# Kernel optimization log

Measured on AMD Instinct MI355X. Metric: run time of the kernel, lower is better.

The kernel has to match this reference:

```python
import jax, jax.numpy as jnp
import numpy as np

IN_FEATURES = 4096
OUT_FEATURES = 4096
SPARSITY = 0.98


def _build_mask():
    # Mirrors _initialize_structured_sparsity: banded deterministic pattern.
    num_connections = int((1 - SPARSITY) * IN_FEATURES * OUT_FEATURES)
    cpn = max(1, num_connections // OUT_FEATURES)  # connections per neuron (=81)
    rows = np.arange(OUT_FEATURES)[:, None]                      # [O,1]
    cols = (rows * cpn + np.arange(cpn)[None, :]) % IN_FEATURES  # [O,cpn]
    mask = np.zeros((OUT_FEATURES, IN_FEATURES), dtype=np.float32)
    mask[np.repeat(np.arange(OUT_FEATURES), cpn), cols.reshape(-1)] = 1.0
    return mask, cpn


def setup_inputs() -> dict:
    key = jax.random.key(0)
    kx, kw = jax.random.split(key)
    mask_np, cpn = _build_mask()
    x = jax.random.normal(kx, (16384, IN_FEATURES), dtype=jnp.float32)
    # weight init: randn * sqrt(2/cpn) at masked positions (dense tensor is fine;
    # forward multiplies by mask anyway, matching the torch module exactly)
    weight = jax.random.normal(kw, (OUT_FEATURES, IN_FEATURES), dtype=jnp.float32) * jnp.float32(np.sqrt(2.0 / cpn))
    bias = jnp.zeros((OUT_FEATURES,), dtype=jnp.float32)
    mask = jnp.asarray(mask_np)
    return {"x": x, "weight": weight, "bias": bias, "mask": mask}


def reference(x, weight, bias, mask):
    # F.linear(x, weight*mask, bias) == x @ (weight*mask).T + bias
    masked_weight = weight * mask  # [O,I]
    return jnp.einsum('bi,oi->bo', x, masked_weight) + bias
```

## Files before the change

### kernel.cpp

```cpp
#include <hip/hip_runtime.h>
#include <hip/hip_bf16.h>

#define IN_F 4096
#define OUT_F 4096
#define CPN 81
#define OINV 2225
#define OB16 2832

#define BMF 8
#define NCH 8
#define CHUNK 512
#define SC4 148
#define XSTR 616
#define RSTRF 8

typedef __attribute__((ext_vector_type(4))) float f32x4;
typedef __attribute__((ext_vector_type(8))) short bf16x8;

__device__ __forceinline__ unsigned short f2bf(float f) {
  __hip_bfloat16 h = __float2bfloat16(f);
  return *reinterpret_cast<unsigned short*>(&h);
}
__device__ __forceinline__ float bf2f(unsigned short u) {
  unsigned int v = ((unsigned int)u) << 16;
  return *reinterpret_cast<float*>(&v);
}

__global__ void prep_wfrag(const float* __restrict__ w,
                           const float* __restrict__ mask,
                           unsigned short* __restrict__ wfrag) {
  int idx = blockIdx.x * 256 + threadIdx.x;
  int lane = idx & 63;
  int t = (idx >> 6) % 3;
  int g = idx / 192;
  int n = lane & 15;
  int kg = lane >> 4;
  int s = g * 16 + n;
  int o = (OINV * s) & 4095;
  unsigned short v8[8];
#pragma unroll
  for (int i = 0; i < 8; ++i) {
    int c = 32 * t + 8 * kg + i;
    int j = c - n;
    float v = 0.f;
    if (j >= 0 && j < CPN) {
      int col = (16 * g + c) & 4095;
      v = w[(size_t)o * IN_F + col] * mask[(size_t)o * IN_F + col];
    }
    v8[i] = f2bf(v);
  }
  *reinterpret_cast<bf16x8*>(wfrag + (size_t)idx * 8) =
      *reinterpret_cast<const bf16x8*>(v8);
}

__global__ __launch_bounds__(512, 4) void sc_fused(
    const float* __restrict__ x, const float* __restrict__ bias,
    const unsigned short* __restrict__ wfrag, float* __restrict__ out) {
  __shared__ unsigned short res[4096 * RSTRF];
  __shared__ unsigned short xl[BMF * XSTR];

  const int blk = blockIdx.x;
  const int b0 = blk * BMF;
  const int tid = threadIdx.x;
  const int wave = tid >> 6;
  const int lane = tid & 63;
  const int ln = lane & 15;
  const int lk = lane >> 4;
  const int oln = (OINV * ln) & 4095;
  const int q0 = blk & 7;

  for (int qq = 0; qq < NCH; ++qq) {
    const int q = (q0 + qq) & 7;
    const int c0 = q * CHUNK;

#pragma unroll
    for (int k = 0; k < 3; ++k) {
      int idx = tid + k * 512;
      if (idx < BMF * SC4) {
        int row = idx / SC4;
        int c4 = idx - row * SC4;
        int col = (c0 + 4 * c4) & 4095;
        const float4 v = *reinterpret_cast<const float4*>(
            x + (size_t)(b0 + row) * IN_F + col);
        ushort4 h;
        h.x = f2bf(v.x); h.y = f2bf(v.y); h.z = f2bf(v.z); h.w = f2bf(v.w);
        *reinterpret_cast<ushort4*>(xl + row * XSTR + 4 * c4) = h;
      }
    }
    __syncthreads();

    const unsigned short* arow = xl + (ln & 7) * XSTR + 8 * lk;
#pragma unroll
    for (int j = 0; j < 4; ++j) {
      const int gl = wave * 4 + j;
      const int g = q * 32 + gl;
      const bf16x8* wf = reinterpret_cast<const bf16x8*>(wfrag)
                       + (size_t)g * 192 + lane;
      const unsigned short* ap = arow + 16 * gl;
      bf16x8 a0 = *reinterpret_cast<const bf16x8*>(ap);
      bf16x8 a1 = *reinterpret_cast<const bf16x8*>(ap + 32);
      bf16x8 a2 = *reinterpret_cast<const bf16x8*>(ap + 64);
      f32x4 acc = f32x4{0.f, 0.f, 0.f, 0.f};
      acc = __builtin_amdgcn_mfma_f32_16x16x32_bf16(a0, wf[0],   acc, 0, 0, 0);
      acc = __builtin_amdgcn_mfma_f32_16x16x32_bf16(a1, wf[64],  acc, 0, 0, 0);
      acc = __builtin_amdgcn_mfma_f32_16x16x32_bf16(a2, wf[128], acc, 0, 0, 0);
      if (lk < 2) {
        int o = (OB16 * g + oln) & 4095;
        ushort4 h;
        h.x = f2bf(acc[0]); h.y = f2bf(acc[1]);
        h.z = f2bf(acc[2]); h.w = f2bf(acc[3]);
        *reinterpret_cast<ushort4*>(res + o * RSTRF + 4 * lk) = h;
      }
    }
    __syncthreads();
  }

  const int h8 = tid >> 8;
  const int c = tid & 255;
#pragma unroll 4
  for (int i = 0; i < 16; ++i) {
    int o = i * 256 + c;
    const uint2 v = *reinterpret_cast<const uint2*>(res + o * RSTRF + 4 * h8);
    float b = bias[o];
    float r0 = bf2f((unsigned short)(v.x & 0xffff)) + b;
    float r1 = bf2f((unsigned short)(v.x >> 16)) + b;
    float r2 = bf2f((unsigned short)(v.y & 0xffff)) + b;
    float r3 = bf2f((unsigned short)(v.y >> 16)) + b;
    size_t base = (size_t)(b0 + 4 * h8) * OUT_F + o;
    out[base]             = r0;
    out[base + OUT_F]     = r1;
    out[base + 2 * OUT_F] = r2;
    out[base + 3 * OUT_F] = r3;
  }
}

extern "C" void kernel_launch(void* const* d_in, const int* in_sizes, int n_in,
                              void* d_out, int out_size, void* d_ws, size_t ws_size,
                              hipStream_t stream) {
  const float* x    = (const float*)d_in[0];
  const float* w    = (const float*)d_in[1];
  const float* bias = (const float*)d_in[2];
  const float* mask = (const float*)d_in[3];
  float* out = (float*)d_out;

  unsigned short* wfrag = (unsigned short*)d_ws;

  const int B = in_sizes[0] / IN_F;

  prep_wfrag<<<192, 256, 0, stream>>>(w, mask, wfrag);
  sc_fused<<<B / BMF, 512, 0, stream>>>(x, bias, wfrag, out);
}
```

Before: 191.1 us.

## Prefetch next x chunk into registers and double-buffer weight fragment loads

Loads the next chunk of x into registers right after the barrier so global latency overlaps the MFMA work, and software-pipelines the weight and LDS fragment loads across the four inner groups. It also changes the epilogue mapping so each wave writes 16 consecutive outputs for pairs of rows instead of 4 rows per thread. This raises register pressure under the 512x4 launch bounds, and the new store pattern writes 16 consecutive floats per row per wave, which may coalesce worse.

```diff
diff --git a/kernel.cpp b/kernel.cpp
--- a/kernel.cpp
+++ b/kernel.cpp
@@ -11,6 +11,7 @@
 #define NCH 8
 #define CHUNK 512
 #define SC4 148
+#define NLD 1184
 #define XSTR 616
 #define RSTRF 8
 
@@ -69,43 +70,75 @@
   const int oln = (OINV * ln) & 4095;
   const int q0 = blk & 7;
 
+  const int i1 = tid + 512, i2 = tid + 1024;
+  const int row0 = tid / SC4, c40 = tid - row0 * SC4;
+  const int row1 = i1  / SC4, c41 = i1  - row1 * SC4;
+  const int row2 = i2  / SC4, c42 = i2  - row2 * SC4;
+  const bool v2 = (i2 < NLD);
+  const float* xp0 = x + (size_t)(b0 + row0) * IN_F;
+  const float* xp1 = x + (size_t)(b0 + row1) * IN_F;
+  const float* xp2 = x + (size_t)(b0 + row2) * IN_F;
+  unsigned short* xw0 = xl + row0 * XSTR + 4 * c40;
+  unsigned short* xw1 = xl + row1 * XSTR + 4 * c41;
+  unsigned short* xw2 = xl + row2 * XSTR + 4 * c42;
+
+  float4 xr0, xr1, xr2;
+  {
+    const int c0 = q0 * CHUNK;
+    xr0 = *reinterpret_cast<const float4*>(xp0 + ((c0 + 4 * c40) & 4095));
+    xr1 = *reinterpret_cast<const float4*>(xp1 + ((c0 + 4 * c41) & 4095));
+    if (v2) xr2 = *reinterpret_cast<const float4*>(xp2 + ((c0 + 4 * c42) & 4095));
+  }
+
   for (int qq = 0; qq < NCH; ++qq) {
     const int q = (q0 + qq) & 7;
-    const int c0 = q * CHUNK;
 
-#pragma unroll
-    for (int k = 0; k < 3; ++k) {
-      int idx = tid + k * 512;
-      if (idx < BMF * SC4) {
-        int row = idx / SC4;
-        int c4 = idx - row * SC4;
-        int col = (c0 + 4 * c4) & 4095;
-        const float4 v = *reinterpret_cast<const float4*>(
-            x + (size_t)(b0 + row) * IN_F + col);
-        ushort4 h;
-        h.x = f2bf(v.x); h.y = f2bf(v.y); h.z = f2bf(v.z); h.w = f2bf(v.w);
-        *reinterpret_cast<ushort4*>(xl + row * XSTR + 4 * c4) = h;
+    {
+      ushort4 h;
+      h.x = f2bf(xr0.x); h.y = f2bf(xr0.y); h.z = f2bf(xr0.z); h.w = f2bf(xr0.w);
+      *reinterpret_cast<ushort4*>(xw0) = h;
+      h.x = f2bf(xr1.x); h.y = f2bf(xr1.y); h.z = f2bf(xr1.z); h.w = f2bf(xr1.w);
+      *reinterpret_cast<ushort4*>(xw1) = h;
+      if (v2) {
+        h.x = f2bf(xr2.x); h.y = f2bf(xr2.y); h.z = f2bf(xr2.z); h.w = f2bf(xr2.w);
+        *reinterpret_cast<ushort4*>(xw2) = h;
       }
     }
     __syncthreads();
 
-    const unsigned short* arow = xl + (ln & 7) * XSTR + 8 * lk;
+    if (qq < NCH - 1) {
+      const int c0n = ((q + 1) & 7) * CHUNK;
+      xr0 = *reinterpret_cast<const float4*>(xp0 + ((c0n + 4 * c40) & 4095));
+      xr1 = *reinterpret_cast<const float4*>(xp1 + ((c0n + 4 * c41) & 4095));
+      if (v2) xr2 = *reinterpret_cast<const float4*>(xp2 + ((c0n + 4 * c42) & 4095));
+    }
+
+    const int gbase = q * 32 + wave * 4;
+    const bf16x8* wf = reinterpret_cast<const bf16x8*>(wfrag)
+                     + (size_t)gbase * 192 + lane;
+    const unsigned short* ap = xl + (ln & 7) * XSTR + 8 * lk + 16 * (wave * 4);
+    bf16x8 nb0 = wf[0], nb1 = wf[64], nb2 = wf[128];
+    bf16x8 na0 = *reinterpret_cast<const bf16x8*>(ap);
+    bf16x8 na1 = *reinterpret_cast<const bf16x8*>(ap + 32);
+    bf16x8 na2 = *reinterpret_cast<const bf16x8*>(ap + 64);
 #pragma unroll
     for (int j = 0; j < 4; ++j) {
-      const int gl = wave * 4 + j;
-      const int g = q * 32 + gl;
-      const bf16x8* wf = reinterpret_cast<const bf16x8*>(wfrag)
-                       + (size_t)g * 192 + lane;
-      const unsigned short* ap = arow + 16 * gl;
-      bf16x8 a0 = *reinterpret_cast<const bf16x8*>(ap);
-      bf16x8 a1 = *reinterpret_cast<const bf16x8*>(ap + 32);
-      bf16x8 a2 = *reinterpret_cast<const bf16x8*>(ap + 64);
+      bf16x8 cb0 = nb0, cb1 = nb1, cb2 = nb2;
+      bf16x8 ca0 = na0, ca1 = na1, ca2 = na2;
+      if (j < 3) {
+        const bf16x8* nwf = wf + (j + 1) * 192;
+        nb0 = nwf[0]; nb1 = nwf[64]; nb2 = nwf[128];
+        const unsigned short* nap = ap + 16 * (j + 1);
+        na0 = *reinterpret_cast<const bf16x8*>(nap);
+        na1 = *reinterpret_cast<const bf16x8*>(nap + 32);
+        na2 = *reinterpret_cast<const bf16x8*>(nap + 64);
+      }
       f32x4 acc = f32x4{0.f, 0.f, 0.f, 0.f};
-      acc = __builtin_amdgcn_mfma_f32_16x16x32_bf16(a0, wf[0],   acc, 0, 0, 0);
-      acc = __builtin_amdgcn_mfma_f32_16x16x32_bf16(a1, wf[64],  acc, 0, 0, 0);
-      acc = __builtin_amdgcn_mfma_f32_16x16x32_bf16(a2, wf[128], acc, 0, 0, 0);
+      acc = __builtin_amdgcn_mfma_f32_16x16x32_bf16(ca0, cb0, acc, 0, 0, 0);
+      acc = __builtin_amdgcn_mfma_f32_16x16x32_bf16(ca1, cb1, acc, 0, 0, 0);
+      acc = __builtin_amdgcn_mfma_f32_16x16x32_bf16(ca2, cb2, acc, 0, 0, 0);
       if (lk < 2) {
-        int o = (OB16 * g + oln) & 4095;
+        int o = (OB16 * (gbase + j) + oln) & 4095;
         ushort4 h;
         h.x = f2bf(acc[0]); h.y = f2bf(acc[1]);
         h.z = f2bf(acc[2]); h.w = f2bf(acc[3]);
@@ -115,22 +148,18 @@
     __syncthreads();
   }
 
-  const int h8 = tid >> 8;
-  const int c = tid & 255;
+  const int j  = lane & 3;
+  const int ol = lane >> 2;
 #pragma unroll 4
-  for (int i = 0; i < 16; ++i) {
-    int o = i * 256 + c;
-    const uint2 v = *reinterpret_cast<const uint2*>(res + o * RSTRF + 4 * h8);
+  for (int it = 0; it < 32; ++it) {
+    int o = it * 128 + wave * 16 + ol;
+    unsigned int v = *reinterpret_cast<const unsigned int*>(res + o * RSTRF + 2 * j);
     float b = bias[o];
-    float r0 = bf2f((unsigned short)(v.x & 0xffff)) + b;
-    float r1 = bf2f((unsigned short)(v.x >> 16)) + b;
-    float r2 = bf2f((unsigned short)(v.y & 0xffff)) + b;
-    float r3 = bf2f((unsigned short)(v.y >> 16)) + b;
-    size_t base = (size_t)(b0 + 4 * h8) * OUT_F + o;
-    out[base]             = r0;
-    out[base + OUT_F]     = r1;
-    out[base + 2 * OUT_F] = r2;
-    out[base + 3 * OUT_F] = r3;
+    float lo = bf2f((unsigned short)(v & 0xffff)) + b;
+    float hi = bf2f((unsigned short)(v >> 16)) + b;
+    size_t base = (size_t)(b0 + 2 * j) * OUT_F + o;
+    out[base]         = lo;
+    out[base + OUT_F] = hi;
   }
 }
 
```

New measurement: 168.1 us. 1.14x faster.
